# Performance work log

Measured on AMD Instinct MI355X. Metric: run time of the kernel, lower is better.

The kernel has to match this reference:

```python
import jax, jax.numpy as jnp
import numpy as np

B, D, H = 16384, 1024, 1024
EPS = 1e-07


def setup_inputs() -> dict:
    key = jax.random.key(0)
    ks = jax.random.split(key, 16)
    s = 1.0 / np.sqrt(D)  # xavier-ish scale keeps exp() gate bounded
    mat = lambda k: (jax.random.normal(k, (D, H), dtype=jnp.float32) * s)
    zeros = lambda: jnp.zeros((H,), dtype=jnp.float32)
    return {
        "x": jax.random.normal(ks[0], (B, D), dtype=jnp.float32),
        "h_prev": jax.random.normal(ks[1], (B, H), dtype=jnp.float32) * 0.1,
        "c_prev": jax.random.normal(ks[2], (B, H), dtype=jnp.float32) * 0.1,
        "n_prev": jnp.ones((B, H), dtype=jnp.float32),
        "Wz": mat(ks[3]), "bWz": zeros(), "Rz": mat(ks[4]), "bRz": zeros(), "bz": zeros(),
        "Wi": mat(ks[5]), "bWi": zeros(), "Ri": mat(ks[6]), "bRi": zeros(), "bi": zeros(),
        "Wf": mat(ks[7]), "bWf": zeros(), "Rf": mat(ks[8]), "bRf": zeros(), "bf": zeros(),
        "Wo": mat(ks[9]), "bWo": zeros(), "Ro": mat(ks[10]), "bRo": zeros(), "bo": zeros(),
        "Wy": mat(ks[11]), "by": jnp.zeros((D,), dtype=jnp.float32),
    }


def reference(x, h_prev, c_prev, n_prev,
              Wz, bWz, Rz, bRz, bz,
              Wi, bWi, Ri, bRi, bi,
              Wf, bWf, Rf, bRf, bf,
              Wo, bWo, Ro, bRo, bo,
              Wy, by):
    # pre-activations: two fused GEMMs via concatenated weights
    Wcat = jnp.concatenate([Wz, Wi, Wf, Wo], axis=1)      # [D, 4H]
    Rcat = jnp.concatenate([Rz, Ri, Rf, Ro], axis=1)      # [H, 4H]
    bcat = jnp.concatenate([bWz + bRz + bz, bWi + bRi + bi,
                            bWf + bRf + bf, bWo + bRo + bo])
    pre = x @ Wcat + h_prev @ Rcat + bcat                  # [B, 4H]
    pz, pi, pf, po = jnp.split(pre, 4, axis=1)
    zt = jnp.tanh(pz)
    it = jnp.exp(pi)
    ft = jax.nn.sigmoid(pf)
    ot = jax.nn.sigmoid(po)
    C = ft * c_prev + it * zt
    n = ft * n_prev + it
    h = ot * jnp.tanh(C / (n + EPS))
    y = h @ Wy + by
    return y, (h, C, n)
```

## Files before the change

### kernel.cpp

```cpp
#include <hip/hip_runtime.h>
#include <math.h>
#include <stdint.h>


typedef __attribute__((ext_vector_type(8))) short bf16x8;
typedef __attribute__((ext_vector_type(4))) float f32x4;

constexpr int Bsz = 16384;
constexpr int Dd  = 1024;
constexpr int Hh  = 1024;
constexpr float EPSv = 1e-7f;

__device__ __forceinline__ unsigned short f2bf(float f) {
    union { float f; uint32_t u; } v; v.f = f;
    uint32_t u = v.u + 0x7fffu + ((v.u >> 16) & 1u);
    return (unsigned short)(u >> 16);
}

__device__ __forceinline__ void gload16(const void* g, void* l) {
    __builtin_amdgcn_global_load_lds(
        (const __attribute__((address_space(1))) void*)g,
        (__attribute__((address_space(3))) void*)l, 16, 0, 0);
}


__global__ __launch_bounds__(256)
void cvt_A(const float* __restrict__ x, const float* __restrict__ hp, unsigned short* __restrict__ A)
{
    const int idx = blockIdx.x * 256 + threadIdx.x;
    const int n = idx * 8;
    const int b = n >> 11, k = n & 2047;
    const float* s = (k < 1024) ? (x + (size_t)b * 1024 + k)
                                : (hp + (size_t)b * 1024 + (k - 1024));
    const float4 v0 = *(const float4*)s;
    const float4 v1 = *(const float4*)(s + 4);
    union { unsigned short u[8]; uint4 v; } pk;
    pk.u[0] = f2bf(v0.x); pk.u[1] = f2bf(v0.y); pk.u[2] = f2bf(v0.z); pk.u[3] = f2bf(v0.w);
    pk.u[4] = f2bf(v1.x); pk.u[5] = f2bf(v1.y); pk.u[6] = f2bf(v1.z); pk.u[7] = f2bf(v1.w);
    *(uint4*)(A + n) = pk.v;
}

__global__ __launch_bounds__(256)
void cvt_T(const float* __restrict__ src, unsigned short* __restrict__ dst,
           int ldd, int kbase, int g, int mode)
{
    __shared__ float tile[64][65];
    const int t = threadIdx.x;
    const int kt = blockIdx.x & 15, jt = blockIdx.x >> 4;
    {
        const int lr = t >> 4, lc = (t & 15) * 4;
        #pragma unroll
        for (int rr = 0; rr < 64; rr += 16) {
            const float4 v = *(const float4*)(src + (size_t)(kt * 64 + rr + lr) * 1024 + jt * 64 + lc);
            tile[rr + lr][lc + 0] = v.x;
            tile[rr + lr][lc + 1] = v.y;
            tile[rr + lr][lc + 2] = v.z;
            tile[rr + lr][lc + 3] = v.w;
        }
    }
    __syncthreads();
    const int jl = t >> 2, kc = (t & 3) * 16;
    const int j = jt * 64 + jl;
    const int cp = mode ? j : ((j & 15) | (g << 4) | ((j >> 4) << 6));
    union { unsigned short u[16]; uint4 v[2]; } pk;
    #pragma unroll
    for (int q = 0; q < 16; ++q) pk.u[q] = f2bf(tile[kc + q][jl]);
    uint4* d = (uint4*)(dst + (size_t)cp * ldd + kbase + kt * 64 + kc);
    d[0] = pk.v[0];
    d[1] = pk.v[1];
}

__global__ __launch_bounds__(256)
void bias_sum(const float* bWz, const float* bRz, const float* bz,
              const float* bWi, const float* bRi, const float* bi,
              const float* bWf, const float* bRf, const float* bf_,
              const float* bWo, const float* bRo, const float* bo,
              float* __restrict__ bs)
{
    const int j = blockIdx.x * 256 + threadIdx.x;
    bs[j]        = bWz[j] + bRz[j] + bz[j];
    bs[1024 + j] = bWi[j] + bRi[j] + bi[j];
    bs[2048 + j] = bWf[j] + bRf[j] + bf_[j];
    bs[3072 + j] = bWo[j] + bRo[j] + bo[j];
}


template<int LDA, int LDB, int KTOT>
__device__ __forceinline__ void mfma8(const unsigned short* __restrict__ Ag,
                                      const unsigned short* __restrict__ Bg,
                                      int m0, int n0, int t,
                                      unsigned short* lds, f32x4 acc[8][4])
{
    constexpr int NT = KTOT / 64;
    constexpr int NI = NT / 2;
    const int lane = t & 63, wid = t >> 6;
    const int wr = wid >> 2, wc = wid & 3;
    const int cl = lane & 15, hi = lane >> 4;
    const int aB = (wr * 128 + cl) * 64 + ((hi ^ (cl & 7)) << 3);
    const int bB = 16384 + (wc * 64 + cl) * 64 + ((hi ^ (cl & 7)) << 3);
    const int srow = t >> 3;
    const int schk = ((t & 7) ^ (srow & 7)) << 3;
    const unsigned short* gA = Ag + (size_t)(m0 + srow) * LDA + schk;
    const unsigned short* gB = Bg + (size_t)(n0 + srow) * LDB + schk;
    unsigned short* ldst = lds + t * 8;

    bf16x8 Ar[4], Br[4][2];

#define STG_A(kt, h, b) { const unsigned short* g_ = gA + (size_t)((h) * 128) * LDA + (kt) * 64; \
    unsigned short* l_ = ldst + (b) * 32768 + (h) * 8192; \
    gload16(g_, l_); gload16(g_ + (size_t)64 * LDA, l_ + 4096); }
#define STG_B(kt, h, b) { const unsigned short* g_ = gB + (size_t)((h) * 128) * LDB + (kt) * 64; \
    unsigned short* l_ = ldst + (b) * 32768 + 16384 + (h) * 8192; \
    gload16(g_, l_); gload16(g_ + (size_t)64 * LDB, l_ + 4096); }
#define RD_A(b, mh, ks) { _Pragma("unroll") for (int mm = 0; mm < 4; ++mm) \
    Ar[mm] = *(const bf16x8*)(lds + (b) * 32768 + ((aB + (mh) * 4096 + mm * 1024) ^ ((ks) * 32))); }
#define RD_B(b, ks) { _Pragma("unroll") for (int nn = 0; nn < 4; ++nn) \
    Br[nn][ks] = *(const bf16x8*)(lds + (b) * 32768 + ((bB + nn * 1024) ^ ((ks) * 32))); }
#define MM(mh, ks) { __builtin_amdgcn_s_setprio(1); \
    _Pragma("unroll") for (int mm = 0; mm < 4; ++mm) \
    _Pragma("unroll") for (int nn = 0; nn < 4; ++nn) \
    acc[(mh) * 4 + mm][nn] = __builtin_amdgcn_mfma_f32_16x16x32_bf16(Ar[mm], Br[nn][ks], acc[(mh) * 4 + mm][nn], 0, 0, 0); \
    __builtin_amdgcn_s_setprio(0); }
#define BAR() __builtin_amdgcn_s_barrier()
#define LGKM0() { asm volatile("s_waitcnt lgkmcnt(0)" ::: "memory"); __builtin_amdgcn_sched_barrier(0); }
#define VMW(n) asm volatile("s_waitcnt vmcnt(" #n ")" ::: "memory")

    STG_B(0, 0, 0); STG_B(0, 1, 0); STG_A(0, 0, 0); STG_A(0, 1, 0);
    STG_B(1, 0, 1); STG_B(1, 1, 1);
    VMW(4); BAR();

    for (int it = 0; it < NI; ++it) {
        const int t1 = 2 * it + 1;
        int t2 = 2 * it + 2; if (t2 >= NT) t2 = NT - 1;
        int t3 = 2 * it + 3; if (t3 >= NT) t3 = NT - 1;
        RD_B(0, 0); RD_A(0, 0, 0); STG_A(t1, 0, 1); BAR(); LGKM0(); MM(0, 0); BAR();
        RD_B(0, 1); RD_A(0, 0, 1); STG_A(t1, 1, 1); BAR(); LGKM0(); MM(0, 1); BAR();
        RD_A(0, 1, 0); STG_B(t2, 0, 0); BAR(); LGKM0(); MM(1, 0); BAR();
        RD_A(0, 1, 1); STG_B(t2, 1, 0); VMW(4); BAR(); LGKM0(); MM(1, 1); BAR();
        RD_B(1, 0); RD_A(1, 0, 0); STG_A(t2, 0, 0); BAR(); LGKM0(); MM(0, 0); BAR();
        RD_B(1, 1); RD_A(1, 0, 1); STG_A(t2, 1, 0); BAR(); LGKM0(); MM(0, 1); BAR();
        RD_A(1, 1, 0); STG_B(t3, 0, 1); BAR(); LGKM0(); MM(1, 0); BAR();
        RD_A(1, 1, 1); STG_B(t3, 1, 1); VMW(4); BAR(); LGKM0(); MM(1, 1); BAR();
    }
    VMW(0);

#undef STG_A
#undef STG_B
#undef RD_A
#undef RD_B
#undef MM
#undef BAR
#undef LGKM0
#undef VMW
}

__global__ __launch_bounds__(512, 2)
void gemm_gates(const unsigned short* __restrict__ A, const unsigned short* __restrict__ WT,
                const float* __restrict__ bsum,
                const float* __restrict__ c_prev, const float* __restrict__ n_prev,
                float* __restrict__ out_h, float* __restrict__ out_C, float* __restrict__ out_n,
                unsigned short* __restrict__ h_bf)
{
    __shared__ unsigned short lds[65536];
    const int t = threadIdx.x;
    const int swz = (blockIdx.x & 7) * 128 + (blockIdx.x >> 3);
    const int mblk = swz & 63, nblk = swz >> 6;
    const int m0 = mblk * 256, n0 = nblk * 256;

    f32x4 acc[8][4];
    #pragma unroll
    for (int i = 0; i < 8; ++i)
        #pragma unroll
        for (int j = 0; j < 4; ++j) acc[i][j] = (f32x4)0.f;

    mfma8<2048, 2048, 2048>(A, WT, m0, n0, t, lds, acc);

    const int lane = t & 63, wid = t >> 6;
    const int wr = wid >> 2, wc = wid & 3;
    const int cl = lane & 15, hi = lane >> 4;
    const int j_out = (nblk * 4 + wc) * 16 + cl;
    const float bz_ = bsum[j_out];
    const float bi_ = bsum[1024 + j_out];
    const float bf_ = bsum[2048 + j_out];
    const float bo_ = bsum[3072 + j_out];
    #pragma unroll
    for (int mf = 0; mf < 8; ++mf) {
        const int rb = m0 + wr * 128 + mf * 16 + hi * 4;
        #pragma unroll
        for (int r = 0; r < 4; ++r) {
            const size_t idx = (size_t)(rb + r) * 1024 + j_out;
            const float pz = acc[mf][0][r] + bz_;
            const float pi = acc[mf][1][r] + bi_;
            const float pf = acc[mf][2][r] + bf_;
            const float po = acc[mf][3][r] + bo_;
            const float zt = tanhf(pz);
            const float it = expf(pi);
            const float ft = 1.f / (1.f + expf(-pf));
            const float ot = 1.f / (1.f + expf(-po));
            const float Cv = ft * c_prev[idx] + it * zt;
            const float nv = ft * n_prev[idx] + it;
            const float hv = ot * tanhf(Cv / (nv + EPSv));
            out_h[idx] = hv;
            out_C[idx] = Cv;
            out_n[idx] = nv;
            h_bf[idx] = f2bf(hv);
        }
    }
}

__global__ __launch_bounds__(512, 2)
void gemm_y(const unsigned short* __restrict__ A, const unsigned short* __restrict__ WyT,
            const float* __restrict__ by, float* __restrict__ y)
{
    __shared__ unsigned short lds[65536];
    const int t = threadIdx.x;
    const int swz = (blockIdx.x & 7) * 32 + (blockIdx.x >> 3);
    const int mblk = swz & 63, nblk = swz >> 6;
    const int m0 = mblk * 256, n0 = nblk * 256;

    f32x4 acc[8][4];
    #pragma unroll
    for (int i = 0; i < 8; ++i)
        #pragma unroll
        for (int j = 0; j < 4; ++j) acc[i][j] = (f32x4)0.f;

    mfma8<1024, 1024, 1024>(A, WyT, m0, n0, t, lds, acc);

    const int lane = t & 63, wid = t >> 6;
    const int wr = wid >> 2, wc = wid & 3;
    const int cl = lane & 15, hi = lane >> 4;
    #pragma unroll
    for (int mf = 0; mf < 8; ++mf) {
        const int rb = m0 + wr * 128 + mf * 16 + hi * 4;
        #pragma unroll
        for (int nf = 0; nf < 4; ++nf) {
            const int c = n0 + wc * 64 + nf * 16 + cl;
            const float bc = by[c];
            #pragma unroll
            for (int r = 0; r < 4; ++r)
                y[(size_t)(rb + r) * 1024 + c] = acc[mf][nf][r] + bc;
        }
    }
}


constexpr int FBM = 64, FBN = 64, FBK = 16, FPAD = 4;

__global__ __launch_bounds__(256)
void fb_gates(const float* __restrict__ x, const float* __restrict__ h_prev,
              const float* __restrict__ c_prev, const float* __restrict__ n_prev,
              const float* __restrict__ Wz, const float* __restrict__ Rz,
              const float* __restrict__ Wi, const float* __restrict__ Ri,
              const float* __restrict__ Wf, const float* __restrict__ Rf,
              const float* __restrict__ Wo, const float* __restrict__ Ro,
              const float* __restrict__ bWz, const float* __restrict__ bRz, const float* __restrict__ bz,
              const float* __restrict__ bWi, const float* __restrict__ bRi, const float* __restrict__ bi,
              const float* __restrict__ bWf, const float* __restrict__ bRf, const float* __restrict__ bf_,
              const float* __restrict__ bWo, const float* __restrict__ bRo, const float* __restrict__ bo,
              float* __restrict__ out_h, float* __restrict__ out_C, float* __restrict__ out_n)
{
    __shared__ float sA[FBK][FBM + FPAD];
    __shared__ float sB[4][FBK][FBN + FPAD];
    const int t = threadIdx.x;
    const int col_blk = blockIdx.x & 15, row_blk = blockIdx.x >> 4;
    const int row0 = row_blk * FBM, col0 = col_blk * FBN;
    const int tx = t & 15, ty = t >> 4;
    float acc[4][4][4];
    #pragma unroll
    for (int g = 0; g < 4; ++g)
        for (int i = 0; i < 4; ++i)
            for (int j = 0; j < 4; ++j) acc[g][i][j] = 0.f;
    const int ar = t >> 2, ak = (t & 3) * 4, wk = t >> 4, wcc = (t & 15) * 4;
    for (int phase = 0; phase < 2; ++phase) {
        const float* Am = phase ? h_prev : x;
        const float* W0 = phase ? Rz : Wz; const float* W1 = phase ? Ri : Wi;
        const float* W2 = phase ? Rf : Wf; const float* W3 = phase ? Ro : Wo;
        for (int k0 = 0; k0 < 1024; k0 += FBK) {
            __syncthreads();
            {
                const float4 v = *(const float4*)(Am + (size_t)(row0 + ar) * 1024 + k0 + ak);
                sA[ak + 0][ar] = v.x; sA[ak + 1][ar] = v.y;
                sA[ak + 2][ar] = v.z; sA[ak + 3][ar] = v.w;
            }
            *(float4*)&sB[0][wk][wcc] = *(const float4*)(W0 + (size_t)(k0 + wk) * 1024 + col0 + wcc);
            *(float4*)&sB[1][wk][wcc] = *(const float4*)(W1 + (size_t)(k0 + wk) * 1024 + col0 + wcc);
            *(float4*)&sB[2][wk][wcc] = *(const float4*)(W2 + (size_t)(k0 + wk) * 1024 + col0 + wcc);
            *(float4*)&sB[3][wk][wcc] = *(const float4*)(W3 + (size_t)(k0 + wk) * 1024 + col0 + wcc);
            __syncthreads();
            #pragma unroll
            for (int kk = 0; kk < FBK; ++kk) {
                float a[4], bb[4][4];
                *(float4*)a = *(const float4*)&sA[kk][ty * 4];
                *(float4*)&bb[0][0] = *(const float4*)&sB[0][kk][tx * 4];
                *(float4*)&bb[1][0] = *(const float4*)&sB[1][kk][tx * 4];
                *(float4*)&bb[2][0] = *(const float4*)&sB[2][kk][tx * 4];
                *(float4*)&bb[3][0] = *(const float4*)&sB[3][kk][tx * 4];
                #pragma unroll
                for (int g = 0; g < 4; ++g)
                    for (int i = 0; i < 4; ++i)
                        for (int j = 0; j < 4; ++j)
                            acc[g][i][j] += a[i] * bb[g][j];
            }
        }
    }
    #pragma unroll
    for (int i = 0; i < 4; ++i) {
        const int r = row0 + ty * 4 + i;
        #pragma unroll
        for (int j = 0; j < 4; ++j) {
            const int c = col0 + tx * 4 + j;
            const float pz = acc[0][i][j] + bWz[c] + bRz[c] + bz[c];
            const float pi = acc[1][i][j] + bWi[c] + bRi[c] + bi[c];
            const float pf = acc[2][i][j] + bWf[c] + bRf[c] + bf_[c];
            const float po = acc[3][i][j] + bWo[c] + bRo[c] + bo[c];
            const float zt = tanhf(pz);
            const float it = expf(pi);
            const float ft = 1.f / (1.f + expf(-pf));
            const float ot = 1.f / (1.f + expf(-po));
            const size_t idx = (size_t)r * Hh + c;
            const float Cv = ft * c_prev[idx] + it * zt;
            const float nv = ft * n_prev[idx] + it;
            out_h[idx] = ot * tanhf(Cv / (nv + EPSv));
            out_C[idx] = Cv;
            out_n[idx] = nv;
        }
    }
}

__global__ __launch_bounds__(256)
void fb_ygemm(const float* __restrict__ hmat, const float* __restrict__ Wy,
              const float* __restrict__ by, float* __restrict__ y)
{
    __shared__ float sA[FBK][FBM + FPAD];
    __shared__ float sB[FBK][FBN + FPAD];
    const int t = threadIdx.x;
    const int col_blk = blockIdx.x & 15, row_blk = blockIdx.x >> 4;
    const int row0 = row_blk * FBM, col0 = col_blk * FBN;
    const int tx = t & 15, ty = t >> 4;
    float acc[4][4];
    #pragma unroll
    for (int i = 0; i < 4; ++i)
        for (int j = 0; j < 4; ++j) acc[i][j] = 0.f;
    const int ar = t >> 2, ak = (t & 3) * 4, wk = t >> 4, wcc = (t & 15) * 4;
    for (int k0 = 0; k0 < 1024; k0 += FBK) {
        __syncthreads();
        {
            const float4 v = *(const float4*)(hmat + (size_t)(row0 + ar) * 1024 + k0 + ak);
            sA[ak + 0][ar] = v.x; sA[ak + 1][ar] = v.y;
            sA[ak + 2][ar] = v.z; sA[ak + 3][ar] = v.w;
        }
        *(float4*)&sB[wk][wcc] = *(const float4*)(Wy + (size_t)(k0 + wk) * 1024 + col0 + wcc);
        __syncthreads();
        #pragma unroll
        for (int kk = 0; kk < FBK; ++kk) {
            float a[4], bb[4];
            *(float4*)a = *(const float4*)&sA[kk][ty * 4];
            *(float4*)bb = *(const float4*)&sB[kk][tx * 4];
            #pragma unroll
            for (int i = 0; i < 4; ++i)
                for (int j = 0; j < 4; ++j)
                    acc[i][j] += a[i] * bb[j];
        }
    }
    #pragma unroll
    for (int i = 0; i < 4; ++i) {
        const int r = row0 + ty * 4 + i;
        #pragma unroll
        for (int j = 0; j < 4; ++j) {
            const int c = col0 + tx * 4 + j;
            y[(size_t)r * Dd + c] = acc[i][j] + by[c];
        }
    }
}


extern "C" void kernel_launch(void* const* d_in, const int* in_sizes, int n_in,
                              void* d_out, int out_size, void* d_ws, size_t ws_size,
                              hipStream_t stream) {
    const float* x      = (const float*)d_in[0];
    const float* h_prev = (const float*)d_in[1];
    const float* c_prev = (const float*)d_in[2];
    const float* n_prev = (const float*)d_in[3];
    const float* Wz  = (const float*)d_in[4];
    const float* bWz = (const float*)d_in[5];
    const float* Rz  = (const float*)d_in[6];
    const float* bRz = (const float*)d_in[7];
    const float* bz  = (const float*)d_in[8];
    const float* Wi  = (const float*)d_in[9];
    const float* bWi = (const float*)d_in[10];
    const float* Ri  = (const float*)d_in[11];
    const float* bRi = (const float*)d_in[12];
    const float* bi  = (const float*)d_in[13];
    const float* Wf  = (const float*)d_in[14];
    const float* bWf = (const float*)d_in[15];
    const float* Rf  = (const float*)d_in[16];
    const float* bRf = (const float*)d_in[17];
    const float* bf_ = (const float*)d_in[18];
    const float* Wo  = (const float*)d_in[19];
    const float* bWo = (const float*)d_in[20];
    const float* Ro  = (const float*)d_in[21];
    const float* bRo = (const float*)d_in[22];
    const float* bo  = (const float*)d_in[23];
    const float* Wy  = (const float*)d_in[24];
    const float* by  = (const float*)d_in[25];

    float* y     = (float*)d_out;
    float* out_h = y + (size_t)Bsz * Dd;
    float* out_C = out_h + (size_t)Bsz * Hh;
    float* out_n = out_C + (size_t)Bsz * Hh;

    const size_t OFF_A    = 0;
    const size_t OFF_WT   = 67108864;
    const size_t OFF_WYT  = 83886080;
    const size_t OFF_HBF  = 85983232;
    const size_t OFF_BS   = 119537664;
    const size_t WS_NEED  = 119554048;

    if (ws_size >= WS_NEED) {
        char* ws = (char*)d_ws;
        unsigned short* A_bf = (unsigned short*)(ws + OFF_A);
        unsigned short* WT   = (unsigned short*)(ws + OFF_WT);
        unsigned short* WyT  = (unsigned short*)(ws + OFF_WYT);
        unsigned short* h_bf = (unsigned short*)(ws + OFF_HBF);
        float* bsum          = (float*)(ws + OFF_BS);

        cvt_A<<<16384, 256, 0, stream>>>(x, h_prev, A_bf);
        cvt_T<<<256, 256, 0, stream>>>(Wz, WT, 2048, 0,    0, 0);
        cvt_T<<<256, 256, 0, stream>>>(Rz, WT, 2048, 1024, 0, 0);
        cvt_T<<<256, 256, 0, stream>>>(Wi, WT, 2048, 0,    1, 0);
        cvt_T<<<256, 256, 0, stream>>>(Ri, WT, 2048, 1024, 1, 0);
        cvt_T<<<256, 256, 0, stream>>>(Wf, WT, 2048, 0,    2, 0);
        cvt_T<<<256, 256, 0, stream>>>(Rf, WT, 2048, 1024, 2, 0);
        cvt_T<<<256, 256, 0, stream>>>(Wo, WT, 2048, 0,    3, 0);
        cvt_T<<<256, 256, 0, stream>>>(Ro, WT, 2048, 1024, 3, 0);
        cvt_T<<<256, 256, 0, stream>>>(Wy, WyT, 1024, 0,   0, 1);
        bias_sum<<<4, 256, 0, stream>>>(bWz, bRz, bz, bWi, bRi, bi,
                                        bWf, bRf, bf_, bWo, bRo, bo, bsum);

        gemm_gates<<<1024, 512, 0, stream>>>(A_bf, WT, bsum, c_prev, n_prev,
                                             out_h, out_C, out_n, h_bf);
        gemm_y<<<256, 512, 0, stream>>>(h_bf, WyT, by, y);
    } else {
        dim3 block(256);
        dim3 grid((Bsz / FBM) * (Hh / FBN));
        fb_gates<<<grid, block, 0, stream>>>(x, h_prev, c_prev, n_prev,
                                             Wz, Rz, Wi, Ri, Wf, Rf, Wo, Ro,
                                             bWz, bRz, bz, bWi, bRi, bi,
                                             bWf, bRf, bf_, bWo, bRo, bo,
                                             out_h, out_C, out_n);
        fb_ygemm<<<grid, block, 0, stream>>>(out_h, Wy, by, y);
    }
}
```

Before: 466.2 us.

## Make gates GEMM persistent over four M tiles with chained K pipeline

Replaces the half-tile staged MFMA loop with a single-stage-per-K-tile double-buffered pipeline that loads full 256-row A/B tiles. The gates GEMM now launches 256 blocks, each looping over four consecutive M tiles with the same N tile, so the B (weight) tile stream continues across output tiles and the epilogue runs between them. The goal is fewer barriers, no pipeline refill between tiles, and a single wave of blocks on the device. The risks are an exposed epilogue inside the mainloop, higher register pressure from holding more A/B fragments, and a reordered block swizzle that may hurt L2 reuse.

```diff
diff --git a/kernel.cpp b/kernel.cpp
--- a/kernel.cpp
+++ b/kernel.cpp
@@ -85,14 +85,13 @@
 }
 
 
-template<int LDA, int LDB, int KTOT>
-__device__ __forceinline__ void mfma8(const unsigned short* __restrict__ Ag,
-                                      const unsigned short* __restrict__ Bg,
-                                      int m0, int n0, int t,
-                                      unsigned short* lds, f32x4 acc[8][4])
-{
-    constexpr int NT = KTOT / 64;
-    constexpr int NI = NT / 2;
+template<int LDA, int NT, int NTILES, class Epi>
+__device__ void mfma_chain(const unsigned short* __restrict__ Ag,
+                           const unsigned short* __restrict__ Bg,
+                           int m0base, int n0, int t,
+                           unsigned short* lds, Epi epi)
+{
+    constexpr int TOT = NT * NTILES;
     const int lane = t & 63, wid = t >> 6;
     const int wr = wid >> 2, wc = wid & 3;
     const int cl = lane & 15, hi = lane >> 4;
@@ -100,58 +99,110 @@
     const int bB = 16384 + (wc * 64 + cl) * 64 + ((hi ^ (cl & 7)) << 3);
     const int srow = t >> 3;
     const int schk = ((t & 7) ^ (srow & 7)) << 3;
-    const unsigned short* gA = Ag + (size_t)(m0 + srow) * LDA + schk;
-    const unsigned short* gB = Bg + (size_t)(n0 + srow) * LDB + schk;
     unsigned short* ldst = lds + t * 8;
 
-    bf16x8 Ar[4], Br[4][2];
-
-#define STG_A(kt, h, b) { const unsigned short* g_ = gA + (size_t)((h) * 128) * LDA + (kt) * 64; \
-    unsigned short* l_ = ldst + (b) * 32768 + (h) * 8192; \
-    gload16(g_, l_); gload16(g_ + (size_t)64 * LDA, l_ + 4096); }
-#define STG_B(kt, h, b) { const unsigned short* g_ = gB + (size_t)((h) * 128) * LDB + (kt) * 64; \
-    unsigned short* l_ = ldst + (b) * 32768 + 16384 + (h) * 8192; \
-    gload16(g_, l_); gload16(g_ + (size_t)64 * LDB, l_ + 4096); }
-#define RD_A(b, mh, ks) { _Pragma("unroll") for (int mm = 0; mm < 4; ++mm) \
-    Ar[mm] = *(const bf16x8*)(lds + (b) * 32768 + ((aB + (mh) * 4096 + mm * 1024) ^ ((ks) * 32))); }
-#define RD_B(b, ks) { _Pragma("unroll") for (int nn = 0; nn < 4; ++nn) \
-    Br[nn][ks] = *(const bf16x8*)(lds + (b) * 32768 + ((bB + nn * 1024) ^ ((ks) * 32))); }
-#define MM(mh, ks) { __builtin_amdgcn_s_setprio(1); \
-    _Pragma("unroll") for (int mm = 0; mm < 4; ++mm) \
-    _Pragma("unroll") for (int nn = 0; nn < 4; ++nn) \
-    acc[(mh) * 4 + mm][nn] = __builtin_amdgcn_mfma_f32_16x16x32_bf16(Ar[mm], Br[nn][ks], acc[(mh) * 4 + mm][nn], 0, 0, 0); \
-    __builtin_amdgcn_s_setprio(0); }
-#define BAR() __builtin_amdgcn_s_barrier()
-#define LGKM0() { asm volatile("s_waitcnt lgkmcnt(0)" ::: "memory"); __builtin_amdgcn_sched_barrier(0); }
-#define VMW(n) asm volatile("s_waitcnt vmcnt(" #n ")" ::: "memory")
-
-    STG_B(0, 0, 0); STG_B(0, 1, 0); STG_A(0, 0, 0); STG_A(0, 1, 0);
-    STG_B(1, 0, 1); STG_B(1, 1, 1);
-    VMW(4); BAR();
-
-    for (int it = 0; it < NI; ++it) {
-        const int t1 = 2 * it + 1;
-        int t2 = 2 * it + 2; if (t2 >= NT) t2 = NT - 1;
-        int t3 = 2 * it + 3; if (t3 >= NT) t3 = NT - 1;
-        RD_B(0, 0); RD_A(0, 0, 0); STG_A(t1, 0, 1); BAR(); LGKM0(); MM(0, 0); BAR();
-        RD_B(0, 1); RD_A(0, 0, 1); STG_A(t1, 1, 1); BAR(); LGKM0(); MM(0, 1); BAR();
-        RD_A(0, 1, 0); STG_B(t2, 0, 0); BAR(); LGKM0(); MM(1, 0); BAR();
-        RD_A(0, 1, 1); STG_B(t2, 1, 0); VMW(4); BAR(); LGKM0(); MM(1, 1); BAR();
-        RD_B(1, 0); RD_A(1, 0, 0); STG_A(t2, 0, 0); BAR(); LGKM0(); MM(0, 0); BAR();
-        RD_B(1, 1); RD_A(1, 0, 1); STG_A(t2, 1, 0); BAR(); LGKM0(); MM(0, 1); BAR();
-        RD_A(1, 1, 0); STG_B(t3, 0, 1); BAR(); LGKM0(); MM(1, 0); BAR();
-        RD_A(1, 1, 1); STG_B(t3, 1, 1); VMW(4); BAR(); LGKM0(); MM(1, 1); BAR();
-    }
-    VMW(0);
-
-#undef STG_A
-#undef STG_B
-#undef RD_A
-#undef RD_B
-#undef MM
-#undef BAR
-#undef LGKM0
-#undef VMW
+    f32x4 acc[8][4];
+    #pragma unroll
+    for (int i = 0; i < 8; ++i)
+        #pragma unroll
+        for (int j = 0; j < 4; ++j) acc[i][j] = (f32x4)0.f;
+
+    auto stgA = [&](int fi, int buf) {
+        const int ot = fi / NT, kt = fi % NT;
+        const unsigned short* g = Ag + (size_t)(m0base + ot * 256 + srow) * LDA + kt * 64 + schk;
+        unsigned short* l = ldst + buf * 32768;
+        gload16(g,                    l);
+        gload16(g + (size_t) 64 * LDA, l + 4096);
+        gload16(g + (size_t)128 * LDA, l + 8192);
+        gload16(g + (size_t)192 * LDA, l + 12288);
+    };
+    auto stgB = [&](int fi, int buf) {
+        const int kt = fi % NT;
+        const unsigned short* g = Bg + (size_t)(n0 + srow) * LDA + kt * 64 + schk;
+        unsigned short* l = ldst + buf * 32768 + 16384;
+        gload16(g,                    l);
+        gload16(g + (size_t) 64 * LDA, l + 4096);
+        gload16(g + (size_t)128 * LDA, l + 8192);
+        gload16(g + (size_t)192 * LDA, l + 12288);
+    };
+
+    stgA(0, 0); stgB(0, 0); stgB(1, 1);
+    asm volatile("s_waitcnt vmcnt(4)" ::: "memory");
+    __builtin_amdgcn_s_barrier();
+
+    for (int fi = 0; fi < TOT; ++fi) {
+        const int bufR = fi & 1;
+        const unsigned short* L = lds + bufR * 32768;
+        int f1 = fi + 1; if (f1 > TOT - 1) f1 = TOT - 1;
+        int f2 = fi + 2; if (f2 > TOT - 1) f2 = TOT - 1;
+
+        bf16x8 Br0[4], Br1[4], Ar00[4], Ar01[4], Ar10[4], Ar11[4];
+        #pragma unroll
+        for (int nn = 0; nn < 4; ++nn) Br0[nn]  = *(const bf16x8*)(L + (bB + nn * 1024));
+        #pragma unroll
+        for (int mm = 0; mm < 4; ++mm) Ar00[mm] = *(const bf16x8*)(L + (aB + mm * 1024));
+
+        stgA(f1, bufR ^ 1);
+
+        #pragma unroll
+        for (int nn = 0; nn < 4; ++nn) Br1[nn]  = *(const bf16x8*)(L + ((bB + nn * 1024) ^ 32));
+        #pragma unroll
+        for (int mm = 0; mm < 4; ++mm) Ar01[mm] = *(const bf16x8*)(L + ((aB + mm * 1024) ^ 32));
+
+        __builtin_amdgcn_s_setprio(1);
+        #pragma unroll
+        for (int mm = 0; mm < 4; ++mm)
+            #pragma unroll
+            for (int nn = 0; nn < 4; ++nn)
+                acc[mm][nn] = __builtin_amdgcn_mfma_f32_16x16x32_bf16(Ar00[mm], Br0[nn], acc[mm][nn], 0, 0, 0);
+        __builtin_amdgcn_s_setprio(0);
+
+        #pragma unroll
+        for (int mm = 0; mm < 4; ++mm) Ar10[mm] = *(const bf16x8*)(L + (aB + 4096 + mm * 1024));
+        #pragma unroll
+        for (int mm = 0; mm < 4; ++mm) Ar11[mm] = *(const bf16x8*)(L + ((aB + 4096 + mm * 1024) ^ 32));
+
+        __builtin_amdgcn_s_setprio(1);
+        #pragma unroll
+        for (int mm = 0; mm < 4; ++mm)
+            #pragma unroll
+            for (int nn = 0; nn < 4; ++nn)
+                acc[mm][nn] = __builtin_amdgcn_mfma_f32_16x16x32_bf16(Ar01[mm], Br1[nn], acc[mm][nn], 0, 0, 0);
+        __builtin_amdgcn_s_setprio(0);
+
+        __builtin_amdgcn_sched_barrier(0);
+        __builtin_amdgcn_s_barrier();
+
+        stgB(f2, bufR);
+
+        __builtin_amdgcn_s_setprio(1);
+        #pragma unroll
+        for (int mm = 0; mm < 4; ++mm)
+            #pragma unroll
+            for (int nn = 0; nn < 4; ++nn)
+                acc[4 + mm][nn] = __builtin_amdgcn_mfma_f32_16x16x32_bf16(Ar10[mm], Br0[nn], acc[4 + mm][nn], 0, 0, 0);
+        __builtin_amdgcn_s_setprio(0);
+        __builtin_amdgcn_s_setprio(1);
+        #pragma unroll
+        for (int mm = 0; mm < 4; ++mm)
+            #pragma unroll
+            for (int nn = 0; nn < 4; ++nn)
+                acc[4 + mm][nn] = __builtin_amdgcn_mfma_f32_16x16x32_bf16(Ar11[mm], Br1[nn], acc[4 + mm][nn], 0, 0, 0);
+        __builtin_amdgcn_s_setprio(0);
+
+        __builtin_amdgcn_sched_barrier(0);
+        asm volatile("s_waitcnt vmcnt(4)" ::: "memory");
+        __builtin_amdgcn_s_barrier();
+
+        if ((fi % NT) == NT - 1) {
+            epi(fi / NT, acc);
+            #pragma unroll
+            for (int i = 0; i < 8; ++i)
+                #pragma unroll
+                for (int j = 0; j < 4; ++j) acc[i][j] = (f32x4)0.f;
+        }
+    }
+    asm volatile("s_waitcnt vmcnt(0)" ::: "memory");
 }
 
 __global__ __launch_bounds__(512, 2)
@@ -163,49 +214,48 @@
 {
     __shared__ unsigned short lds[65536];
     const int t = threadIdx.x;
-    const int swz = (blockIdx.x & 7) * 128 + (blockIdx.x >> 3);
-    const int mblk = swz & 63, nblk = swz >> 6;
-    const int m0 = mblk * 256, n0 = nblk * 256;
-
-    f32x4 acc[8][4];
-    #pragma unroll
-    for (int i = 0; i < 8; ++i)
-        #pragma unroll
-        for (int j = 0; j < 4; ++j) acc[i][j] = (f32x4)0.f;
-
-    mfma8<2048, 2048, 2048>(A, WT, m0, n0, t, lds, acc);
+    const int b = blockIdx.x;
+    const int nb  = (b & 7) * 2 + (b >> 7);
+    const int mb0 = ((b >> 3) & 15) * 4;
+    const int m0base = mb0 * 256;
+    const int n0 = nb * 256;
 
     const int lane = t & 63, wid = t >> 6;
     const int wr = wid >> 2, wc = wid & 3;
     const int cl = lane & 15, hi = lane >> 4;
-    const int j_out = (nblk * 4 + wc) * 16 + cl;
+    const int j_out = nb * 64 + wc * 16 + cl;
     const float bz_ = bsum[j_out];
     const float bi_ = bsum[1024 + j_out];
     const float bf_ = bsum[2048 + j_out];
     const float bo_ = bsum[3072 + j_out];
-    #pragma unroll
-    for (int mf = 0; mf < 8; ++mf) {
-        const int rb = m0 + wr * 128 + mf * 16 + hi * 4;
-        #pragma unroll
-        for (int r = 0; r < 4; ++r) {
-            const size_t idx = (size_t)(rb + r) * 1024 + j_out;
-            const float pz = acc[mf][0][r] + bz_;
-            const float pi = acc[mf][1][r] + bi_;
-            const float pf = acc[mf][2][r] + bf_;
-            const float po = acc[mf][3][r] + bo_;
-            const float zt = tanhf(pz);
-            const float it = expf(pi);
-            const float ft = 1.f / (1.f + expf(-pf));
-            const float ot = 1.f / (1.f + expf(-po));
-            const float Cv = ft * c_prev[idx] + it * zt;
-            const float nv = ft * n_prev[idx] + it;
-            const float hv = ot * tanhf(Cv / (nv + EPSv));
-            out_h[idx] = hv;
-            out_C[idx] = Cv;
-            out_n[idx] = nv;
-            h_bf[idx] = f2bf(hv);
-        }
-    }
+
+    auto epi = [&](int ot, f32x4 (&acc)[8][4]) {
+        #pragma unroll
+        for (int mf = 0; mf < 8; ++mf) {
+            const int rb = m0base + ot * 256 + wr * 128 + mf * 16 + hi * 4;
+            #pragma unroll
+            for (int r = 0; r < 4; ++r) {
+                const size_t idx = (size_t)(rb + r) * 1024 + j_out;
+                const float pz = acc[mf][0][r] + bz_;
+                const float pi = acc[mf][1][r] + bi_;
+                const float pf = acc[mf][2][r] + bf_;
+                const float po = acc[mf][3][r] + bo_;
+                const float zt = tanhf(pz);
+                const float it = expf(pi);
+                const float ft = 1.f / (1.f + expf(-pf));
+                const float ot_ = 1.f / (1.f + expf(-po));
+                const float Cv = ft * c_prev[idx] + it * zt;
+                const float nv = ft * n_prev[idx] + it;
+                const float hv = ot_ * tanhf(Cv / (nv + EPSv));
+                out_h[idx] = hv;
+                out_C[idx] = Cv;
+                out_n[idx] = nv;
+                h_bf[idx] = f2bf(hv);
+            }
+        }
+    };
+
+    mfma_chain<2048, 32, 4>(A, WT, m0base, n0, t, lds, epi);
 }
 
 __global__ __launch_bounds__(512, 2)
@@ -214,33 +264,31 @@
 {
     __shared__ unsigned short lds[65536];
     const int t = threadIdx.x;
-    const int swz = (blockIdx.x & 7) * 32 + (blockIdx.x >> 3);
-    const int mblk = swz & 63, nblk = swz >> 6;
-    const int m0 = mblk * 256, n0 = nblk * 256;
-
-    f32x4 acc[8][4];
-    #pragma unroll
-    for (int i = 0; i < 8; ++i)
-        #pragma unroll
-        for (int j = 0; j < 4; ++j) acc[i][j] = (f32x4)0.f;
-
-    mfma8<1024, 1024, 1024>(A, WyT, m0, n0, t, lds, acc);
+    const int b = blockIdx.x;
+    const int nb = b & 3, mb = b >> 2;
+    const int m0base = mb * 256, n0 = nb * 256;
 
     const int lane = t & 63, wid = t >> 6;
     const int wr = wid >> 2, wc = wid & 3;
     const int cl = lane & 15, hi = lane >> 4;
-    #pragma unroll
-    for (int mf = 0; mf < 8; ++mf) {
-        const int rb = m0 + wr * 128 + mf * 16 + hi * 4;
-        #pragma unroll
-        for (int nf = 0; nf < 4; ++nf) {
-            const int c = n0 + wc * 64 + nf * 16 + cl;
-            const float bc = by[c];
-            #pragma unroll
-            for (int r = 0; r < 4; ++r)
-                y[(size_t)(rb + r) * 1024 + c] = acc[mf][nf][r] + bc;
-        }
-    }
+
+    auto epi = [&](int ot, f32x4 (&acc)[8][4]) {
+        (void)ot;
+        #pragma unroll
+        for (int mf = 0; mf < 8; ++mf) {
+            const int rb = m0base + wr * 128 + mf * 16 + hi * 4;
+            #pragma unroll
+            for (int nf = 0; nf < 4; ++nf) {
+                const int c = n0 + wc * 64 + nf * 16 + cl;
+                const float bc = by[c];
+                #pragma unroll
+                for (int r = 0; r < 4; ++r)
+                    y[(size_t)(rb + r) * 1024 + c] = acc[mf][nf][r] + bc;
+            }
+        }
+    };
+
+    mfma_chain<1024, 16, 1>(A, WyT, m0base, n0, t, lds, epi);
 }
 
 
@@ -437,8 +485,8 @@
         bias_sum<<<4, 256, 0, stream>>>(bWz, bRz, bz, bWi, bRi, bi,
                                         bWf, bRf, bf_, bWo, bRo, bo, bsum);
 
-        gemm_gates<<<1024, 512, 0, stream>>>(A_bf, WT, bsum, c_prev, n_prev,
-                                             out_h, out_C, out_n, h_bf);
+        gemm_gates<<<256, 512, 0, stream>>>(A_bf, WT, bsum, c_prev, n_prev,
+                                            out_h, out_C, out_n, h_bf);
         gemm_y<<<256, 512, 0, stream>>>(h_bf, WyT, by, y);
     } else {
         dim3 block(256);
```

Result: faster. 451.4 us (-3.2%).
